# Kernel tuning notes

Hardware: AMD Instinct MI355X
Metric: run time of the kernel (lower is better)

Reference implementation:

```python
import jax, jax.numpy as jnp
import numpy as np

B, S, D, N, HD, M = 2, 2048, 1024, 16, 64, 4096  # batch, seq, d_model, heads, head_dim, d_mlp


def setup_inputs() -> dict:
    key = jax.random.key(0)
    ks = jax.random.split(key, 8)
    sd = 1.0 / np.sqrt(D)
    return {
        "x": jax.random.normal(ks[0], (B, S, D), dtype=jnp.float32),
        "W_qkv": jax.random.normal(ks[1], (N, D, 3 * HD), dtype=jnp.float32) * sd,
        "W_out": jax.random.normal(ks[2], (N, HD, D), dtype=jnp.float32) * sd,
        "ln1_w": jnp.ones((D,), jnp.float32),
        "ln1_b": jnp.zeros((D,), jnp.float32),
        "ln2_w": jnp.ones((D,), jnp.float32),
        "ln2_b": jnp.zeros((D,), jnp.float32),
        "W1": jax.random.normal(ks[3], (D, M), dtype=jnp.float32) * sd,
        "b1": jnp.zeros((M,), jnp.float32),
        "W2": jax.random.normal(ks[4], (M, D), dtype=jnp.float32) / np.sqrt(M),
        "b2": jnp.zeros((D,), jnp.float32),
    }


def _layernorm(x, w, b, eps=1e-4):
    mu = jnp.mean(x, axis=-1, keepdims=True)
    var = jnp.var(x, axis=-1, keepdims=True, ddof=1)  # torch unbiased var
    return w * (x - mu) / jnp.sqrt(var + eps) + b


def _attention(x, W_qkv, W_out):
    b, s, d = x.shape
    qkv = jnp.einsum('bsd,ndh->bnsh', x, W_qkv)  # [b,n,s,3*hd]
    q, k, v = jnp.split(qkv, 3, axis=-1)
    hd = q.shape[-1]
    attn = jnp.einsum('bnqh,bnkh->bnqk', q, k) / np.sqrt(hd)
    mask = -1e10 * (1.0 - jnp.tril(jnp.ones((s, s), jnp.float32)))
    attn = jax.nn.softmax(attn + mask, axis=-1)
    out = jnp.einsum('bnqk,bnkh->bnqh', attn, v)  # [b,n,s,hd]
    # faithful to torch: raw memory reinterpretation (b,n,s,hd) -> (b, n*hd, s)
    out = out.reshape(b, -1, s)
    # faithful to torch: d is a shared free index -> W_out summed over (n,h)
    out = jnp.einsum('bds,nhd->bsd', out, W_out)
    return out


def _mlp(x, W1, b1, W2, b2):
    h = jax.nn.gelu(x @ W1 + b1, approximate=False)
    return h @ W2 + b2


def reference(x, W_qkv, W_out, ln1_w, ln1_b, ln2_w, ln2_b, W1, b1, W2, b2):
    x = x + _attention(_layernorm(x, ln1_w, ln1_b), W_qkv, W_out)
    x = x + _mlp(_layernorm(x, ln2_w, ln2_b), W1, b1, W2, b2)
    return x
```

## Files before the change

### kernel.cpp

```cpp
#include <hip/hip_runtime.h>

typedef unsigned short ushort_t;
typedef __attribute__((ext_vector_type(8))) short short8;
typedef __attribute__((ext_vector_type(4))) float floatx4;
typedef __attribute__((ext_vector_type(4))) unsigned short ushort4v;

#define B_ 2
#define S_ 2048
#define D_ 1024
#define NH_ 16
#define HD_ 64
#define M_ 4096

#define KSCALE 0.18033688011112042f

__device__ __forceinline__ ushort_t f2bf(float f) {
    unsigned u = __builtin_bit_cast(unsigned, f);
    return (ushort_t)((u + 0x7FFFu + ((u >> 16) & 1u)) >> 16);
}

__device__ __forceinline__ void gload_lds16(const ushort_t* g, ushort_t* l) {
    __builtin_amdgcn_global_load_lds(
        (const __attribute__((address_space(1))) unsigned int*)(g),
        (__attribute__((address_space(3))) unsigned int*)(l), 16, 0, 0);
}

__device__ __forceinline__ ushort_t to_bf_elem(float f) { return f2bf(f); }
__device__ __forceinline__ ushort_t to_bf_elem(ushort_t u) { return u; }

template <typename T>
__global__ __launch_bounds__(256) void transpose_to_bf16(
    const T* __restrict__ src, ushort_t* __restrict__ dst,
    int R, int C, long sbatch, long dbatch, int srs, int drs) {
    __shared__ ushort_t tile[32][33];
    src += (size_t)blockIdx.z * sbatch;
    dst += (size_t)blockIdx.z * dbatch;
    int c = blockIdx.x * 32 + threadIdx.x;
    #pragma unroll
    for (int i = 0; i < 4; ++i) {
        int r = blockIdx.y * 32 + threadIdx.y + i * 8;
        if (r < R && c < C) tile[threadIdx.y + i * 8][threadIdx.x] = to_bf_elem(src[(size_t)r * srs + c]);
    }
    __syncthreads();
    int rr = blockIdx.y * 32 + threadIdx.x;
    #pragma unroll
    for (int i = 0; i < 4; ++i) {
        int cc = blockIdx.x * 32 + threadIdx.y + i * 8;
        if (cc < C && rr < R) dst[(size_t)cc * drs + rr] = tile[threadIdx.x][threadIdx.y + i * 8];
    }
}

__global__ __launch_bounds__(256) void wsum_kernel(const float* __restrict__ W_out,
                                                   float* __restrict__ wsum) {
    int col = blockIdx.x * 32 + (threadIdx.x & 31);
    int rg = threadIdx.x >> 5;
    float s = 0.f;
    for (int r = rg; r < NH_ * HD_; r += 8) s += W_out[(size_t)r * D_ + col];
    __shared__ float part[256];
    part[threadIdx.x] = s;
    __syncthreads();
    if (threadIdx.x < 32) {
        float t = 0.f;
        #pragma unroll
        for (int g = 0; g < 8; ++g) t += part[g * 32 + threadIdx.x];
        wsum[blockIdx.x * 32 + threadIdx.x] = t;
    }
}

__global__ __launch_bounds__(256) void ln1_kernel(const float* __restrict__ x,
                                                  const float* __restrict__ w,
                                                  const float* __restrict__ b,
                                                  ushort_t* __restrict__ out) {
    int row = blockIdx.x, tid = threadIdx.x;
    float v[4], s = 0.f, ss = 0.f;
    #pragma unroll
    for (int i = 0; i < 4; ++i) {
        v[i] = x[(size_t)row * D_ + tid + i * 256];
        s += v[i]; ss += v[i] * v[i];
    }
    #pragma unroll
    for (int off = 32; off >= 1; off >>= 1) { s += __shfl_xor(s, off); ss += __shfl_xor(ss, off); }
    __shared__ float red[8];
    if ((tid & 63) == 0) { red[(tid >> 6) * 2] = s; red[(tid >> 6) * 2 + 1] = ss; }
    __syncthreads();
    s = red[0] + red[2] + red[4] + red[6];
    ss = red[1] + red[3] + red[5] + red[7];
    float mu = s * (1.f / D_);
    float var = (ss - (float)D_ * mu * mu) * (1.f / (D_ - 1));
    float rstd = rsqrtf(var + 1e-4f);
    #pragma unroll
    for (int i = 0; i < 4; ++i) {
        int d = tid + i * 256;
        out[(size_t)row * D_ + d] = f2bf((v[i] - mu) * rstd * w[d] + b[d]);
    }
}

__global__ __launch_bounds__(256) void resid_ln2_kernel(
    const float* __restrict__ x, const float* __restrict__ attn,
    const float* __restrict__ wsum, const float* __restrict__ w,
    const float* __restrict__ b, float* __restrict__ x1, ushort_t* __restrict__ out) {
    int row = blockIdx.x;
    int bb = row >> 11, sidx = row & 2047;
    int tid = threadIdx.x;
    float v[4], s = 0.f, ss = 0.f;
    #pragma unroll
    for (int i = 0; i < 4; ++i) {
        int d = tid + i * 256;
        int n = d >> 6;
        int sp = ((d & 63) << 5) + (sidx >> 6);
        int h = sidx & 63;
        float a = attn[(((size_t)bb * NH_ + n) * S_ + sp) * HD_ + h];
        float val = x[(size_t)row * D_ + d] + wsum[d] * a;
        x1[(size_t)row * D_ + d] = val;
        v[i] = val; s += val; ss += val * val;
    }
    #pragma unroll
    for (int off = 32; off >= 1; off >>= 1) { s += __shfl_xor(s, off); ss += __shfl_xor(ss, off); }
    __shared__ float red[8];
    if ((tid & 63) == 0) { red[(tid >> 6) * 2] = s; red[(tid >> 6) * 2 + 1] = ss; }
    __syncthreads();
    s = red[0] + red[2] + red[4] + red[6];
    ss = red[1] + red[3] + red[5] + red[7];
    float mu = s * (1.f / D_);
    float var = (ss - (float)D_ * mu * mu) * (1.f / (D_ - 1));
    float rstd = rsqrtf(var + 1e-4f);
    #pragma unroll
    for (int i = 0; i < 4; ++i) {
        int d = tid + i * 256;
        out[(size_t)row * D_ + d] = f2bf((v[i] - mu) * rstd * w[d] + b[d]);
    }
}

template <int EPI>
__global__ __launch_bounds__(256) void gemm_bt(
    const ushort_t* __restrict__ A, const ushort_t* __restrict__ BT,
    int M, int N, int K, int ld, const float* __restrict__ bias,
    const float* __restrict__ resid, void* __restrict__ outp) {
    __shared__ __align__(16) ushort_t As[128 * 64];
    __shared__ __align__(16) ushort_t Bs[128 * 64];
    const int tid = threadIdx.x;
    const int lane = tid & 63, wave = tid >> 6;
    const int ln15 = lane & 15, qd = lane >> 4;
    const int wm = wave >> 1, wn = wave & 1;
    const int bm = blockIdx.y, bn = blockIdx.x;
    const int lr = lane >> 3;
    const int sw = (lane & 7) ^ lr;
    if (EPI == 3) {
        A += (size_t)blockIdx.z * K;
        BT += (size_t)blockIdx.z * K;
    }

    floatx4 acc[4][4];
    #pragma unroll
    for (int i = 0; i < 4; ++i)
        #pragma unroll
        for (int j = 0; j < 4; ++j) acc[i][j] = (floatx4){0.f, 0.f, 0.f, 0.f};

    for (int k0 = 0; k0 < K; k0 += 64) {
        __syncthreads();
        #pragma unroll
        for (int l = 0; l < 4; ++l) {
            int r0 = (l * 4 + wave) * 8;
            gload_lds16(A + (size_t)(bm * 128 + r0 + lr) * ld + k0 + sw * 8, &As[r0 * 64]);
            gload_lds16(BT + (size_t)(bn * 128 + r0 + lr) * ld + k0 + sw * 8, &Bs[r0 * 64]);
        }
        __syncthreads();
        #pragma unroll
        for (int ks = 0; ks < 2; ++ks) {
            short8 a[4], b[4];
            #pragma unroll
            for (int mt = 0; mt < 4; ++mt) {
                int row = wm * 64 + mt * 16 + ln15;
                a[mt] = *(const short8*)&As[row * 64 + (((ks * 4 + qd) ^ (row & 7)) << 3)];
            }
            #pragma unroll
            for (int nt = 0; nt < 4; ++nt) {
                int row = wn * 64 + nt * 16 + ln15;
                b[nt] = *(const short8*)&Bs[row * 64 + (((ks * 4 + qd) ^ (row & 7)) << 3)];
            }
            #pragma unroll
            for (int mt = 0; mt < 4; ++mt)
                #pragma unroll
                for (int nt = 0; nt < 4; ++nt)
                    acc[mt][nt] = __builtin_amdgcn_mfma_f32_16x16x32_bf16(a[mt], b[nt], acc[mt][nt], 0, 0, 0);
        }
    }

    const int row0 = bm * 128 + wm * 64, col0 = bn * 128 + wn * 64;
    #pragma unroll
    for (int mt = 0; mt < 4; ++mt)
        #pragma unroll
        for (int nt = 0; nt < 4; ++nt)
            #pragma unroll
            for (int r = 0; r < 4; ++r) {
                int row = row0 + mt * 16 + qd * 4 + r;
                int col = col0 + nt * 16 + ln15;
                float v = acc[mt][nt][r];
                if (EPI == 0) {
                    int bb = row >> 11, sidx = row & 2047;
                    unsigned uc = (unsigned)col;
                    unsigned hn = uc / 192u;
                    unsigned j = uc - hn * 192u;
                    if (j >= 64u && j < 128u) v *= KSCALE;
                    ((ushort_t*)outp)[(((size_t)bb * NH_ + hn) * S_ + sidx) * 192 + j] = f2bf(v);
                } else if (EPI == 1) {
                    v += bias[col];
                    float g = 0.5f * v * (1.0f + erff(v * 0.70710678118654752f));
                    ((ushort_t*)outp)[(size_t)row * N + col] = f2bf(g);
                } else if (EPI == 2) {
                    v += bias[col] + resid[(size_t)row * N + col];
                    ((float*)outp)[(size_t)row * N + col] = v;
                } else {
                    float* po = (float*)outp + (size_t)blockIdx.z * M * N;
                    po[(size_t)row * N + col] = v;
                }
            }
}

__global__ __launch_bounds__(256) void mlp2_reduce(const float* __restrict__ part,
                                                   const float* __restrict__ b2,
                                                   const float* __restrict__ x1,
                                                   float* __restrict__ out) {
    const size_t NTOT = (size_t)B_ * S_ * D_;
    size_t i = ((size_t)blockIdx.x * 256 + threadIdx.x) * 4;
    floatx4 s = *(const floatx4*)(part + i);
    s += *(const floatx4*)(part + NTOT + i);
    s += *(const floatx4*)(part + 2 * NTOT + i);
    s += *(const floatx4*)(part + 3 * NTOT + i);
    int col = (int)(i & (D_ - 1));
    s += *(const floatx4*)(b2 + col);
    s += *(const floatx4*)(x1 + i);
    *(floatx4*)(out + i) = s;
}

__global__ __launch_bounds__(256) void attn_kernel(const ushort_t* __restrict__ qkv,
                                                   const ushort_t* __restrict__ vT,
                                                   float* __restrict__ attn_out) {
    __shared__ __align__(16) ushort_t Ks[64 * 64];
    __shared__ __align__(16) ushort_t Vs[64 * 64];
    __shared__ __align__(16) ushort_t Ps[4][16 * 72];
    const int tid = threadIdx.x, lane = tid & 63, w = tid >> 6;
    const int ln15 = lane & 15, qd = lane >> 4;
    const int qt = (int)gridDim.x - 1 - (int)blockIdx.x;
    const int bh = blockIdx.z * NH_ + blockIdx.y;
    const int qb = qt * 64 + w * 16;
    const size_t qbase = (size_t)bh * S_ * 192;
    const size_t vtbase = (size_t)bh * HD_ * S_;
    ushort_t* myP = (ushort_t*)Ps[w];

    const ushort_t* qrow = qkv + qbase + (size_t)(qb + ln15) * 192;
    short8 bq[2];
    bq[0] = *(const short8*)(qrow + qd * 8);
    bq[1] = *(const short8*)(qrow + 32 + qd * 8);

    float lcur = 0.f;
    floatx4 oacc[4];
    #pragma unroll
    for (int mt = 0; mt < 4; ++mt) oacc[mt] = (floatx4){0.f, 0.f, 0.f, 0.f};

    for (int kt = 0; kt <= qt; ++kt) {
        __syncthreads();
        #pragma unroll
        for (int i = 0; i < 2; ++i) {
            int gb = (i * 4 + w) * 64;
            int g = gb + lane;
            int row = g >> 3, cg = (g & 7) ^ (row & 7);
            gload_lds16(qkv + qbase + (size_t)(kt * 64 + row) * 192 + 64 + cg * 8, &Ks[gb * 8]);
            gload_lds16(vT + vtbase + (size_t)row * S_ + kt * 64 + cg * 8, &Vs[gb * 8]);
        }
        __syncthreads();

        floatx4 sacc[4];
        #pragma unroll
        for (int mt = 0; mt < 4; ++mt) sacc[mt] = (floatx4){0.f, 0.f, 0.f, 0.f};
        #pragma unroll
        for (int ks = 0; ks < 2; ++ks)
            #pragma unroll
            for (int mt = 0; mt < 4; ++mt) {
                int row = mt * 16 + ln15;
                short8 ak = *(const short8*)&Ks[row * 64 + (((ks * 4 + qd) ^ (row & 7)) << 3)];
                sacc[mt] = __builtin_amdgcn_mfma_f32_16x16x32_bf16(ak, bq[ks], sacc[mt], 0, 0, 0);
            }
        if (kt == qt) {
            int q = qb + ln15;
            #pragma unroll
            for (int mt = 0; mt < 4; ++mt)
                #pragma unroll
                for (int r = 0; r < 4; ++r)
                    if (kt * 64 + mt * 16 + qd * 4 + r > q) sacc[mt][r] = -1e30f;
        }
        float rsum = 0.f;
        #pragma unroll
        for (int mt = 0; mt < 4; ++mt) {
            ushort4v pk;
            #pragma unroll
            for (int r = 0; r < 4; ++r) {
                float p = exp2f(sacc[mt][r]);
                rsum += p;
                pk[r] = (ushort_t)(__builtin_bit_cast(unsigned, p) >> 16);
            }
            *(ushort4v*)&myP[ln15 * 72 + mt * 16 + qd * 4] = pk;
        }
        rsum += __shfl_xor(rsum, 16);
        rsum += __shfl_xor(rsum, 32);
        lcur += rsum;
        #pragma unroll
        for (int g = 0; g < 2; ++g) {
            short8 bp = *(const short8*)&myP[ln15 * 72 + g * 32 + qd * 8];
            #pragma unroll
            for (int mt = 0; mt < 4; ++mt) {
                int row = mt * 16 + ln15;
                short8 av = *(const short8*)&Vs[row * 64 + (((g * 4 + qd) ^ (row & 7)) << 3)];
                oacc[mt] = __builtin_amdgcn_mfma_f32_16x16x32_bf16(av, bp, oacc[mt], 0, 0, 0);
            }
        }
    }
    float inv = 1.f / lcur;
    int q = qb + ln15;
    #pragma unroll
    for (int mt = 0; mt < 4; ++mt) {
        floatx4 o = oacc[mt] * inv;
        *(floatx4*)&attn_out[((size_t)bh * S_ + q) * HD_ + mt * 16 + qd * 4] = o;
    }
}

extern "C" void kernel_launch(void* const* d_in, const int* in_sizes, int n_in,
                              void* d_out, int out_size, void* d_ws, size_t ws_size,
                              hipStream_t stream) {
    const float* x = (const float*)d_in[0];
    const float* W_qkv = (const float*)d_in[1];
    const float* W_out = (const float*)d_in[2];
    const float* ln1_w = (const float*)d_in[3];
    const float* ln1_b = (const float*)d_in[4];
    const float* ln2_w = (const float*)d_in[5];
    const float* ln2_b = (const float*)d_in[6];
    const float* W1 = (const float*)d_in[7];
    const float* b1 = (const float*)d_in[8];
    const float* W2 = (const float*)d_in[9];
    const float* b2 = (const float*)d_in[10];

    char* ws = (char*)d_ws;
    const size_t MB = 1024 * 1024;
    ushort_t* ln1_out = (ushort_t*)(ws + 0 * MB);
    ushort_t* WqkvT   = (ushort_t*)(ws + 8 * MB);
    ushort_t* qkv     = (ushort_t*)(ws + 14 * MB);
    ushort_t* vT      = (ushort_t*)(ws + 38 * MB);
    float*    attn_o  = (float*)(ws + 46 * MB);
    float*    partials = (float*)(ws + 0 * MB);
    float*    x1      = (float*)(ws + 64 * MB);
    ushort_t* ln2_out = (ushort_t*)(ws + 80 * MB);
    ushort_t* W1T     = (ushort_t*)(ws + 88 * MB);
    ushort_t* hbuf    = (ushort_t*)(ws + 96 * MB);
    ushort_t* W2T     = (ushort_t*)(ws + 128 * MB);
    float*    wsum    = (float*)(ws + 136 * MB);

    dim3 tb(32, 8);
    transpose_to_bf16<float><<<dim3(192 / 32, D_ / 32, NH_), tb, 0, stream>>>(
        W_qkv, WqkvT, D_, 192, (long)D_ * 192, (long)192 * D_, 192, D_);
    transpose_to_bf16<float><<<dim3(M_ / 32, D_ / 32, 1), tb, 0, stream>>>(
        W1, W1T, D_, M_, 0, 0, M_, D_);
    transpose_to_bf16<float><<<dim3(D_ / 32, M_ / 32, 1), tb, 0, stream>>>(
        W2, W2T, M_, D_, 0, 0, D_, M_);
    wsum_kernel<<<dim3(D_ / 32), 256, 0, stream>>>(W_out, wsum);
    ln1_kernel<<<dim3(B_ * S_), 256, 0, stream>>>(x, ln1_w, ln1_b, ln1_out);
    gemm_bt<0><<<dim3(3072 / 128, (B_ * S_) / 128), 256, 0, stream>>>(
        ln1_out, WqkvT, B_ * S_, 3072, D_, D_, nullptr, nullptr, qkv);
    transpose_to_bf16<ushort_t><<<dim3(HD_ / 32, S_ / 32, B_ * NH_), tb, 0, stream>>>(
        qkv + 128, vT, S_, HD_, (long)S_ * 192, (long)HD_ * S_, 192, S_);
    attn_kernel<<<dim3(S_ / 64, NH_, B_), 256, 0, stream>>>(qkv, vT, attn_o);
    resid_ln2_kernel<<<dim3(B_ * S_), 256, 0, stream>>>(x, attn_o, wsum, ln2_w, ln2_b, x1, ln2_out);
    gemm_bt<1><<<dim3(M_ / 128, (B_ * S_) / 128), 256, 0, stream>>>(
        ln2_out, W1T, B_ * S_, M_, D_, D_, b1, nullptr, hbuf);
    gemm_bt<3><<<dim3(D_ / 128, (B_ * S_) / 128, 4), 256, 0, stream>>>(
        hbuf, W2T, B_ * S_, D_, M_ / 4, M_, nullptr, nullptr, partials);
    mlp2_reduce<<<dim3((B_ * S_ * D_) / 1024), 256, 0, stream>>>(partials, b2, x1, (float*)d_out);
}
```

Measured before the change: 468.7 us.

## Process two key tiles per attention sync and gather attention output via LDS tile

The attention kernel now loads 128 keys of K and V per barrier pair and runs two 64-key compute sub-steps between syncs, which halves synchronization and load-issue rounds. Out-of-range keys are clamped and skipped. The fused residual+LN2 kernel is split into a tiled gather kernel that transposes the strided attention output through shared memory for coalesced reads, followed by a reuse of the LN kernel on x1. This adds an extra kernel launch and an extra read of x1 in exchange for coalesced access.

```diff
diff --git a/kernel.cpp b/kernel.cpp
--- a/kernel.cpp
+++ b/kernel.cpp
@@ -95,39 +95,32 @@
     }
 }
 
-__global__ __launch_bounds__(256) void resid_ln2_kernel(
+__global__ __launch_bounds__(256) void gather_resid(
     const float* __restrict__ x, const float* __restrict__ attn,
-    const float* __restrict__ wsum, const float* __restrict__ w,
-    const float* __restrict__ b, float* __restrict__ x1, ushort_t* __restrict__ out) {
-    int row = blockIdx.x;
-    int bb = row >> 11, sidx = row & 2047;
-    int tid = threadIdx.x;
-    float v[4], s = 0.f, ss = 0.f;
-    #pragma unroll
-    for (int i = 0; i < 4; ++i) {
-        int d = tid + i * 256;
-        int n = d >> 6;
-        int sp = ((d & 63) << 5) + (sidx >> 6);
-        int h = sidx & 63;
-        float a = attn[(((size_t)bb * NH_ + n) * S_ + sp) * HD_ + h];
-        float val = x[(size_t)row * D_ + d] + wsum[d] * a;
-        x1[(size_t)row * D_ + d] = val;
-        v[i] = val; s += val; ss += val * val;
-    }
-    #pragma unroll
-    for (int off = 32; off >= 1; off >>= 1) { s += __shfl_xor(s, off); ss += __shfl_xor(ss, off); }
-    __shared__ float red[8];
-    if ((tid & 63) == 0) { red[(tid >> 6) * 2] = s; red[(tid >> 6) * 2 + 1] = ss; }
+    const float* __restrict__ wsum, float* __restrict__ x1) {
+    __shared__ float tile[128][65];
+    const int tid = threadIdx.x;
+    const int dchunk = blockIdx.x;
+    const int stile = blockIdx.y;
+    const int b = stile >> 5, shi = stile & 31;
+    const int h = tid & 63;
+    const int wv = tid >> 6;
+    #pragma unroll
+    for (int r = 0; r < 32; ++r) {
+        int dloc = r * 4 + wv;
+        int d = dchunk * 128 + dloc;
+        int q = ((d & 63) << 5) + shi;
+        tile[dloc][h] = attn[((size_t)(b * NH_ + (d >> 6)) * S_ + q) * HD_ + h];
+    }
     __syncthreads();
-    s = red[0] + red[2] + red[4] + red[6];
-    ss = red[1] + red[3] + red[5] + red[7];
-    float mu = s * (1.f / D_);
-    float var = (ss - (float)D_ * mu * mu) * (1.f / (D_ - 1));
-    float rstd = rsqrtf(var + 1e-4f);
-    #pragma unroll
-    for (int i = 0; i < 4; ++i) {
-        int d = tid + i * 256;
-        out[(size_t)row * D_ + d] = f2bf((v[i] - mu) * rstd * w[d] + b[d]);
+    const int row0 = b * S_ + shi * 64;
+    #pragma unroll
+    for (int r = 0; r < 32; ++r) {
+        int sr = r * 2 + (tid >> 7);
+        int dcol = tid & 127;
+        int d = dchunk * 128 + dcol;
+        size_t idx = (size_t)(row0 + sr) * D_ + d;
+        x1[idx] = x[idx] + wsum[d] * tile[dcol][sr];
     }
 }
 
@@ -236,8 +229,8 @@
 __global__ __launch_bounds__(256) void attn_kernel(const ushort_t* __restrict__ qkv,
                                                    const ushort_t* __restrict__ vT,
                                                    float* __restrict__ attn_out) {
-    __shared__ __align__(16) ushort_t Ks[64 * 64];
-    __shared__ __align__(16) ushort_t Vs[64 * 64];
+    __shared__ __align__(16) ushort_t Ks[128 * 64];
+    __shared__ __align__(16) ushort_t Vs[64 * 128];
     __shared__ __align__(16) ushort_t Ps[4][16 * 72];
     const int tid = threadIdx.x, lane = tid & 63, w = tid >> 6;
     const int ln15 = lane & 15, qd = lane >> 4;
@@ -258,60 +251,69 @@
     #pragma unroll
     for (int mt = 0; mt < 4; ++mt) oacc[mt] = (floatx4){0.f, 0.f, 0.f, 0.f};
 
-    for (int kt = 0; kt <= qt; ++kt) {
+    const int ntiles = qt + 1;
+    for (int kt2 = 0; kt2 < ntiles; kt2 += 2) {
         __syncthreads();
         #pragma unroll
-        for (int i = 0; i < 2; ++i) {
+        for (int i = 0; i < 4; ++i) {
             int gb = (i * 4 + w) * 64;
             int g = gb + lane;
-            int row = g >> 3, cg = (g & 7) ^ (row & 7);
-            gload_lds16(qkv + qbase + (size_t)(kt * 64 + row) * 192 + 64 + cg * 8, &Ks[gb * 8]);
-            gload_lds16(vT + vtbase + (size_t)row * S_ + kt * 64 + cg * 8, &Vs[gb * 8]);
+            int krow = g >> 3;
+            int kcg = (g & 7) ^ (krow & 7);
+            int key = kt2 * 64 + krow; if (key > S_ - 1) key = S_ - 1;
+            gload_lds16(qkv + qbase + (size_t)key * 192 + 64 + kcg * 8, &Ks[gb * 8]);
+            int vrow = g >> 4;
+            int vcg = (g & 15) ^ (vrow & 15);
+            int vkey = kt2 * 64 + vcg * 8; if (vkey > S_ - 8) vkey = S_ - 8;
+            gload_lds16(vT + vtbase + (size_t)vrow * S_ + vkey, &Vs[gb * 8]);
         }
         __syncthreads();
 
-        floatx4 sacc[4];
-        #pragma unroll
-        for (int mt = 0; mt < 4; ++mt) sacc[mt] = (floatx4){0.f, 0.f, 0.f, 0.f};
-        #pragma unroll
-        for (int ks = 0; ks < 2; ++ks)
+        int nk = ntiles - kt2; if (nk > 2) nk = 2;
+        for (int kh = 0; kh < nk; ++kh) {
+            floatx4 sacc[4];
+            #pragma unroll
+            for (int mt = 0; mt < 4; ++mt) sacc[mt] = (floatx4){0.f, 0.f, 0.f, 0.f};
+            #pragma unroll
+            for (int ks = 0; ks < 2; ++ks)
+                #pragma unroll
+                for (int mt = 0; mt < 4; ++mt) {
+                    int row = kh * 64 + mt * 16 + ln15;
+                    short8 ak = *(const short8*)&Ks[row * 64 + (((ks * 4 + qd) ^ (row & 7)) << 3)];
+                    sacc[mt] = __builtin_amdgcn_mfma_f32_16x16x32_bf16(ak, bq[ks], sacc[mt], 0, 0, 0);
+                }
+            if (kt2 + kh == qt) {
+                int q = qb + ln15;
+                #pragma unroll
+                for (int mt = 0; mt < 4; ++mt)
+                    #pragma unroll
+                    for (int r = 0; r < 4; ++r)
+                        if (qt * 64 + mt * 16 + qd * 4 + r > q) sacc[mt][r] = -1e30f;
+            }
+            float rsum = 0.f;
             #pragma unroll
             for (int mt = 0; mt < 4; ++mt) {
-                int row = mt * 16 + ln15;
-                short8 ak = *(const short8*)&Ks[row * 64 + (((ks * 4 + qd) ^ (row & 7)) << 3)];
-                sacc[mt] = __builtin_amdgcn_mfma_f32_16x16x32_bf16(ak, bq[ks], sacc[mt], 0, 0, 0);
-            }
-        if (kt == qt) {
-            int q = qb + ln15;
-            #pragma unroll
-            for (int mt = 0; mt < 4; ++mt)
-                #pragma unroll
-                for (int r = 0; r < 4; ++r)
-                    if (kt * 64 + mt * 16 + qd * 4 + r > q) sacc[mt][r] = -1e30f;
-        }
-        float rsum = 0.f;
-        #pragma unroll
-        for (int mt = 0; mt < 4; ++mt) {
-            ushort4v pk;
-            #pragma unroll
-            for (int r = 0; r < 4; ++r) {
-                float p = exp2f(sacc[mt][r]);
-                rsum += p;
-                pk[r] = (ushort_t)(__builtin_bit_cast(unsigned, p) >> 16);
-            }
-            *(ushort4v*)&myP[ln15 * 72 + mt * 16 + qd * 4] = pk;
-        }
-        rsum += __shfl_xor(rsum, 16);
-        rsum += __shfl_xor(rsum, 32);
-        lcur += rsum;
-        #pragma unroll
-        for (int g = 0; g < 2; ++g) {
-            short8 bp = *(const short8*)&myP[ln15 * 72 + g * 32 + qd * 8];
-            #pragma unroll
-            for (int mt = 0; mt < 4; ++mt) {
-                int row = mt * 16 + ln15;
-                short8 av = *(const short8*)&Vs[row * 64 + (((g * 4 + qd) ^ (row & 7)) << 3)];
-                oacc[mt] = __builtin_amdgcn_mfma_f32_16x16x32_bf16(av, bp, oacc[mt], 0, 0, 0);
+                ushort4v pk;
+                #pragma unroll
+                for (int r = 0; r < 4; ++r) {
+                    float p = exp2f(sacc[mt][r]);
+                    rsum += p;
+                    pk[r] = (ushort_t)(__builtin_bit_cast(unsigned, p) >> 16);
+                }
+                *(ushort4v*)&myP[ln15 * 72 + mt * 16 + qd * 4] = pk;
+            }
+            rsum += __shfl_xor(rsum, 16);
+            rsum += __shfl_xor(rsum, 32);
+            lcur += rsum;
+            #pragma unroll
+            for (int g2 = 0; g2 < 2; ++g2) {
+                short8 bp = *(const short8*)&myP[ln15 * 72 + g2 * 32 + qd * 8];
+                #pragma unroll
+                for (int mt = 0; mt < 4; ++mt) {
+                    int row = mt * 16 + ln15;
+                    short8 av = *(const short8*)&Vs[row * 128 + (((kh * 8 + g2 * 4 + qd) ^ (row & 15)) << 3)];
+                    oacc[mt] = __builtin_amdgcn_mfma_f32_16x16x32_bf16(av, bp, oacc[mt], 0, 0, 0);
+                }
             }
         }
     }
@@ -368,7 +370,8 @@
     transpose_to_bf16<ushort_t><<<dim3(HD_ / 32, S_ / 32, B_ * NH_), tb, 0, stream>>>(
         qkv + 128, vT, S_, HD_, (long)S_ * 192, (long)HD_ * S_, 192, S_);
     attn_kernel<<<dim3(S_ / 64, NH_, B_), 256, 0, stream>>>(qkv, vT, attn_o);
-    resid_ln2_kernel<<<dim3(B_ * S_), 256, 0, stream>>>(x, attn_o, wsum, ln2_w, ln2_b, x1, ln2_out);
+    gather_resid<<<dim3(8, 64), 256, 0, stream>>>(x, attn_o, wsum, x1);
+    ln1_kernel<<<dim3(B_ * S_), 256, 0, stream>>>(x1, ln2_w, ln2_b, ln2_out);
     gemm_bt<1><<<dim3(M_ / 128, (B_ * S_) / 128), 256, 0, stream>>>(
         ln2_out, W1T, B_ * S_, M_, D_, D_, b1, nullptr, hbuf);
     gemm_bt<3><<<dim3(D_ / 128, (B_ * S_) / 128, 4), 256, 0, stream>>>(
```

Measured after the change: 445.7 us. -4.9%, faster.
